# Kernel tuning notes

Hardware: AMD Instinct MI355X
Metric: run time of the kernel (lower is better)

The kernel has to match this reference:

```python
import jax, jax.numpy as jnp
import numpy as np

EMB, GCN = 256, 256
N_REL = 200
B, E, TOPK = 256, 100000, 64
N_PREV, N_ENT, N_TIME = 50000, 20000, 2000


def _linear(x, w, b):
    # torch nn.Linear convention: w is [out, in]
    return x @ w.T + b


def setup_inputs() -> dict:
    key = jax.random.key(0)
    ks = jax.random.split(key, 32)
    nrm = lambda k, s: (jax.random.normal(k, s, jnp.float32) * 0.05)
    # facts columns: b, n, h, r, t, ts. b built so every batch has >= TOPK facts.
    b_col = jax.random.permutation(ks[0], jnp.arange(E, dtype=jnp.int32) % B)
    n_col = jax.random.randint(ks[1], (E,), 0, N_PREV, jnp.int32)
    h_col = jax.random.randint(ks[2], (E,), 0, N_ENT, jnp.int32)
    r_col = jax.random.randint(ks[3], (E,), 0, N_REL, jnp.int32)  # r+1 indexes [zero;rel]
    t_col = jax.random.randint(ks[4], (E,), 0, N_ENT, jnp.int32)
    ts_col = jax.random.randint(ks[5], (E,), 0, N_TIME, jnp.int32)
    facts = jnp.stack([b_col, n_col, h_col, r_col, t_col, ts_col], axis=1)
    return {
        "query_time": jax.random.randint(ks[6], (B,), 0, N_TIME, jnp.int32),  # unused by forward
        "query_emd": nrm(ks[7], (B, EMB)),
        "temp_neighbors_facts": facts,
        "ent_emd": nrm(ks[8], (N_ENT, GCN)),
        "rel_emd": nrm(ks[9], (N_REL, GCN)),
        "hidden_node": nrm(ks[10], (N_PREV, EMB)),
        "hidden_rel": nrm(ks[11], (N_PREV, EMB)),
        "hidden_time": nrm(ks[12], (N_PREV, EMB)),  # unused by forward
        "att_agg": jax.random.uniform(ks[13], (N_PREV,), jnp.float32),
        "time_emd": nrm(ks[14], (N_TIME, EMB)),
        "zero_rel_emd": nrm(ks[15], (1, GCN)),
        "W_message_w": nrm(ks[16], (EMB, 2 * EMB)), "W_message_b": jnp.zeros((EMB,), jnp.float32),
        "att_1_w": nrm(ks[17], (1, 3 * EMB)), "att_1_b": jnp.zeros((1,), jnp.float32),
        "att_2_w": nrm(ks[18], (1, EMB)), "att_2_b": jnp.zeros((1,), jnp.float32),
        "W_h_w": nrm(ks[19], (EMB, 2 * EMB)), "W_h_b": jnp.zeros((EMB,), jnp.float32),
        "lin_e_ts_w": nrm(ks[20], (EMB, GCN + EMB)), "lin_e_ts_b": jnp.zeros((EMB,), jnp.float32),
        "lin_r_ts_w": nrm(ks[21], (EMB, GCN)), "lin_r_ts_b": jnp.zeros((EMB,), jnp.float32),
        "lin_time_w": nrm(ks[22], (EMB, EMB)), "lin_time_b": jnp.zeros((EMB,), jnp.float32),
        "gru_w_ih": nrm(ks[23], (3 * EMB, EMB)), "gru_w_hh": nrm(ks[24], (3 * EMB, EMB)),
        "gru_b_ih": jnp.zeros((3 * EMB,), jnp.float32), "gru_b_hh": jnp.zeros((3 * EMB,), jnp.float32),
        "batch_size": B, "device": 0, "max_nodes": TOPK,
    }


def reference(query_time, query_emd, temp_neighbors_facts, ent_emd, rel_emd,
              hidden_node, hidden_rel, hidden_time, att_agg, time_emd,
              zero_rel_emd, W_message_w, W_message_b, att_1_w, att_1_b,
              att_2_w, att_2_b, W_h_w, W_h_b, lin_e_ts_w, lin_e_ts_b,
              lin_r_ts_w, lin_r_ts_b, lin_time_w, lin_time_b,
              gru_w_ih, gru_w_hh, gru_b_ih, gru_b_hh,
              batch_size, device, max_nodes):
    f = temp_neighbors_facts
    b, n, r, t, ts = f[:, 0], f[:, 1], f[:, 3], f[:, 4], f[:, 5]

    hidden_node_pre = hidden_node[n]            # [E, EMB]
    hidden_rel_pre = hidden_rel[n]              # [E, EMB]
    rel_all = jnp.concatenate([zero_rel_emd, rel_emd], axis=0)
    h_r = rel_all[r + 1]                        # [E, GCN]
    h_ts_raw = time_emd[ts]                     # [E, EMB]
    h_t = _linear(jnp.concatenate([ent_emd[t], h_ts_raw], -1), lin_e_ts_w, lin_e_ts_b)
    h_r = _linear(h_r, lin_r_ts_w, lin_r_ts_b)
    _ = _linear(h_ts_raw, lin_time_w, lin_time_b)  # computed but unused in original

    message = _linear(jnp.concatenate([hidden_node_pre, h_r], -1), W_message_w, W_message_b)
    att_input = jnp.concatenate([query_emd[b], message, h_t], -1)  # [E, 3*EMB]
    att1 = jax.nn.sigmoid(_linear(att_input, att_1_w, att_1_b))[:, 0]

    # single-step GRU (torch nn.GRU gate math)
    gi = h_r @ gru_w_ih.T + gru_b_ih            # [E, 3*EMB]
    gh = hidden_rel_pre @ gru_w_hh.T + gru_b_hh
    i_r, i_z, i_n = jnp.split(gi, 3, axis=-1)
    h_rg, h_zg, h_ng = jnp.split(gh, 3, axis=-1)
    rg = jax.nn.sigmoid(i_r + h_rg)
    zg = jax.nn.sigmoid(i_z + h_zg)
    ng = jnp.tanh(i_n + rg * h_ng)
    hidden_rel_new = (1.0 - zg) * ng + zg * hidden_rel_pre

    att2 = jax.nn.sigmoid(_linear(hidden_rel_new, att_2_w, att_2_b))[:, 0]
    attention = (att1 + att2) * 0.5

    # vectorized per-batch top-k (each batch is guaranteed >= max_nodes facts)
    order = jnp.lexsort((-attention, b))        # sort by batch asc, attention desc
    counts = jax.ops.segment_sum(jnp.ones_like(b), b, num_segments=batch_size)
    starts = jnp.cumsum(counts) - counts
    sel = (starts[:, None] + jnp.arange(max_nodes)[None, :]).reshape(-1)
    new_index = order[sel]                      # [B*topk]

    facts_k = f[new_index]
    message = message[new_index]
    hidden_rel_new = hidden_rel_new[new_index]
    attention = (att1[new_index] + att2[new_index]) * 0.5
    b_k, n_k = facts_k[:, 0], facts_k[:, 1]
    attention = attention * att_agg[n_k]
    M = b_k.shape[0]

    rows = facts_k[:, jnp.array([0, 4, 5])]     # (b, t, ts)
    tail_nodes, tail_index = jnp.unique(rows, axis=0, size=M, fill_value=0, return_inverse=True)
    tail_index = tail_index.reshape(-1)

    tail_emd = _linear(jnp.concatenate([ent_emd[tail_nodes[:, 1]], time_emd[tail_nodes[:, 2]]], -1),
                       lin_e_ts_w, lin_e_ts_b)

    # group_max_norm: normalize attention by per-batch sum (0/0 -> 0)
    den = jax.ops.segment_sum(attention, b_k, num_segments=batch_size)[b_k]
    safe_den = jnp.where(den != 0, den, 1.0)
    attention = jnp.where(den != 0, attention / safe_den, 0.0)

    message_agg = jax.ops.segment_sum(attention[:, None] * message, tail_index, num_segments=M)
    hidden_node_new = _linear(jnp.concatenate([message_agg, tail_emd], -1), W_h_w, W_h_b)  # act = identity
    hidden_rel_out = jax.ops.segment_sum(attention[:, None] * hidden_rel_new, tail_index, num_segments=M)
    att_agg_new = jax.ops.segment_sum(attention, tail_index, num_segments=M)
    return tail_nodes, hidden_node_new, hidden_rel_out, att_agg_new
```

## Files before the change

kernel.cpp:

```cpp
#include <hip/hip_runtime.h>
#include <hip/hip_bf16.h>

#define E_N    100000
#define B_N    256
#define TOPK   64
#define NPREV  50000
#define NENT   20000
#define NTIME  2000
#define NREL   200
#define M_OUT  16384
#define NT8    6250

static __device__ __forceinline__ float sigm(float x){ return 1.f/(1.f+expf(-x)); }

__global__ void zero_kernel(unsigned* __restrict__ p, int n){
  int i = blockIdx.x*256 + threadIdx.x;
  if (i < n) p[i] = 0u;
}

__global__ void pack_w_kernel(const float* __restrict__ w_msg,
                              const float* __restrict__ w_hh,
                              const float* __restrict__ lets_w,
                              const float* __restrict__ w_h,
                              float4* __restrict__ wP,
                              float4* __restrict__ wPL,
                              float4* __restrict__ wPH){
  int i = blockIdx.x*256 + threadIdx.x;
  if (i < 65536){
    int t = i & 255, mat = (i >> 8) & 3, kblk = i >> 10;
    float4 v;
    if (mat == 0) v = *(const float4*)&w_msg[(size_t)t*512 + kblk*4];
    else          v = *(const float4*)&w_hh[(size_t)((mat-1)*256 + t)*256 + kblk*4];
    wP[i] = v;
  } else if (i < 98304){
    int j = i - 65536;
    int t = j & 255, mat = (j >> 8) & 1, kblk = j >> 9;
    wPL[j] = *(const float4*)&lets_w[(size_t)t*512 + mat*256 + kblk*4];
  } else if (i < 131072){
    int j = i - 98304;
    int t = j & 255, kblk = j >> 8;
    wPH[j] = *(const float4*)&w_h[(size_t)t*512 + kblk*4];
  }
}

__global__ void matvec_fused(const float* __restrict__ w_msg,
                             const float* __restrict__ lets_w,
                             const float* __restrict__ lets_b,
                             const float* __restrict__ att1w,
                             const float* __restrict__ att1b,
                             float* __restrict__ wm1a, float* __restrict__ ve,
                             float* __restrict__ vts, float* __restrict__ consts){
  int blk = blockIdx.x, t = threadIdx.x;
  if (blk == 3){
    if (t < 64){
      float p = 0.f;
      for (int d = t; d < 256; d += 64) p += lets_b[d]*att1w[512+d];
      for (int o = 32; o > 0; o >>= 1) p += __shfl_down(p, o);
      if (t == 0) consts[0] = att1b[0] + p;
    }
    return;
  }
  const float* M; int moff; const float* v; float* out;
  if (blk == 0){ M = w_msg;  moff = 0;   v = att1w+256; out = wm1a; }
  else if (blk == 1){ M = lets_w; moff = 0;   v = att1w+512; out = ve; }
  else { M = lets_w; moff = 256; v = att1w+512; out = vts; }
  float acc = 0.f;
  #pragma unroll 8
  for (int d = 0; d < 256; ++d) acc += M[(size_t)d*512 + moff + t] * v[d];
  out[t] = acc;
}

__global__ void rows_dot_multi(
    const float* __restrict__ A0, const float* __restrict__ v0, float* __restrict__ o0, int n0,
    const float* __restrict__ A1, const float* __restrict__ v1, float* __restrict__ o1_, int n1,
    const float* __restrict__ A2, const float* __restrict__ v2, float* __restrict__ o2, int n2,
    const float* __restrict__ A3, const float* __restrict__ v3, float* __restrict__ o3, int n3,
    const float* __restrict__ A4, const float* __restrict__ v4, float* __restrict__ o4, int n4){
  int gid = blockIdx.x*256 + threadIdx.x;
  int wid = gid >> 6, lane = gid & 63;
  const float* A; const float* v; float* o; int r;
  if (wid < n0){ A=A0; v=v0; o=o0; r=wid; }
  else if ((wid -= n0) < n1){ A=A1; v=v1; o=o1_; r=wid; }
  else if ((wid -= n1) < n2){ A=A2; v=v2; o=o2; r=wid; }
  else if ((wid -= n2) < n3){ A=A3; v=v3; o=o3; r=wid; }
  else if ((wid -= n3) < n4){ A=A4; v=v4; o=o4; r=wid; }
  else return;
  const float* row = A + (size_t)r*256;
  float p = 0.f;
  for (int k = lane; k < 256; k += 64) p += row[k]*v[k];
  for (int off = 32; off > 0; off >>= 1) p += __shfl_down(p, off);
  if (lane == 0) o[r] = p;
}

template<int ND>
__global__ __launch_bounds__(256) void tile_linear(
    const float* __restrict__ A, int lda,
    const float* __restrict__ Bw, int ldb, int boff,
    const float* __restrict__ bias,
    float* __restrict__ out, int ldo, int rows){
  __shared__ float a_s[16][260];
  int tile0 = blockIdx.x*16;
  for (int idx = threadIdx.x; idx < 16*256; idx += 256){
    int i = idx >> 8, k = idx & 255;
    int row = tile0 + i;
    a_s[i][k] = (row < rows) ? A[(size_t)row*lda + k] : 0.f;
  }
  __syncthreads();
  int d = threadIdx.x;
  const float* brow[ND];
  #pragma unroll
  for (int q = 0; q < ND; ++q) brow[q] = Bw + (size_t)(d + 256*q)*ldb + boff;
  float acc[ND][16];
  #pragma unroll
  for (int q = 0; q < ND; ++q){
    float bv = bias ? bias[d + 256*q] : 0.f;
    #pragma unroll
    for (int i = 0; i < 16; ++i) acc[q][i] = bv;
  }
  for (int k = 0; k < 256; k += 4){
    float4 w[ND];
    #pragma unroll
    for (int q = 0; q < ND; ++q) w[q] = *(const float4*)(brow[q] + k);
    #pragma unroll
    for (int i = 0; i < 16; ++i){
      float4 a = *(const float4*)&a_s[i][k];
      #pragma unroll
      for (int q = 0; q < ND; ++q)
        acc[q][i] += w[q].x*a.x + w[q].y*a.y + w[q].z*a.z + w[q].w*a.w;
    }
  }
  #pragma unroll
  for (int i = 0; i < 16; ++i){
    int row = tile0 + i;
    if (row < rows){
      #pragma unroll
      for (int q = 0; q < ND; ++q) out[(size_t)row*ldo + d + 256*q] = acc[q][i];
    }
  }
}

__global__ __launch_bounds__(256) void gemv_ets2(
    const float* __restrict__ ent_emd, const float* __restrict__ time_emd,
    const float4* __restrict__ wPL, const float* __restrict__ lets_b,
    float* __restrict__ ent_t, float* __restrict__ time_t){
  int blk = blockIdx.x, t = threadIdx.x;
  const float* act; float* out; int matsel, tile0; float bv;
  if (blk < NENT/16){
    act = ent_emd; out = ent_t; matsel = 0; tile0 = blk*16; bv = lets_b[t];
  } else {
    act = time_emd; out = time_t; matsel = 1; tile0 = (blk - NENT/16)*16; bv = 0.f;
  }
  float acc[16];
  #pragma unroll
  for (int p = 0; p < 16; ++p) acc[p] = bv;
  float4 w = wPL[matsel*256 + t];
  for (int kb = 0; kb < 64; ++kb){
    int kbn = (kb + 1) & 63;
    float4 nw = wPL[(kbn*2 + matsel)*256 + t];
    int k = kb*4;
    #pragma unroll
    for (int p = 0; p < 16; ++p){
      float4 a = *(const float4*)&act[(size_t)(tile0+p)*256 + k];
      acc[p] += w.x*a.x + w.y*a.y + w.z*a.z + w.w*a.w;
    }
    w = nw;
  }
  #pragma unroll
  for (int p = 0; p < 16; ++p)
    out[(size_t)(tile0+p)*256 + t] = acc[p];
}

__global__ void hist2_kernel(const int* __restrict__ facts,
                             int* __restrict__ cnt_t, int* __restrict__ cnt_b){
  int e = blockIdx.x*256 + threadIdx.x;
  if (e < E_N){
    atomicAdd(&cnt_t[facts[e*6+1] >> 3], 1);
    atomicAdd(&cnt_b[facts[e*6+0]], 1);
  }
}

__global__ __launch_bounds__(256) void scan2_lds(
    const int* __restrict__ cnt_t, int* __restrict__ off_t, int* __restrict__ cur_t,
    const int* __restrict__ cnt_b, int* __restrict__ off_b, int* __restrict__ cur_b){
  __shared__ int buf[6272];
  __shared__ int sums[256];
  int t = threadIdx.x;
  int c0 = t*25, c1 = c0 + 25; if (c1 > NT8) c1 = NT8; if (c0 > NT8) c0 = NT8;
  int s = 0;
  for (int i = c0; i < c1; ++i){ buf[i] = s; s += cnt_t[i]; }
  sums[t] = s;
  __syncthreads();
  for (int o = 1; o < 256; o <<= 1){
    int v = (t >= o) ? sums[t-o] : 0;
    __syncthreads();
    sums[t] += v;
    __syncthreads();
  }
  int add = (t == 0) ? 0 : sums[t-1];
  for (int i = c0; i < c1; ++i){ int v = buf[i] + add; off_t[i] = v; cur_t[i] = v; }
  if (t == 0) off_t[NT8] = E_N;
  __syncthreads();
  int orig = cnt_b[t];
  sums[t] = orig;
  __syncthreads();
  for (int o = 1; o < 256; o <<= 1){
    int v = (t >= o) ? sums[t-o] : 0;
    __syncthreads();
    sums[t] += v;
    __syncthreads();
  }
  int ex = sums[t] - orig;
  off_b[t] = ex; cur_b[t] = ex;
  if (t == 0) off_b[B_N] = E_N;
}

__global__ void scatter2_kernel(const int* __restrict__ facts,
                                int* __restrict__ cur_t, int* __restrict__ edges_t,
                                int* __restrict__ cur_b, int* __restrict__ edges_b){
  int e = blockIdx.x*256 + threadIdx.x;
  if (e < E_N){
    int pt = atomicAdd(&cur_t[facts[e*6+1] >> 3], 1);
    edges_t[pt] = e;
    int pb = atomicAdd(&cur_b[facts[e*6+0]], 1);
    edges_b[pb] = e;
  }
}

__global__ __launch_bounds__(256) void att_kernel(
    const float* __restrict__ hidden_rel,
    const float4* __restrict__ wP,
    const float* __restrict__ b_hh,
    const float* __restrict__ gi,
    const float* __restrict__ att2w, const float* __restrict__ att2b,
    const int* __restrict__ facts,
    const int* __restrict__ bin_off, const int* __restrict__ bin_edges,
    const float* __restrict__ qdot, const float* __restrict__ sn_m,
    const float* __restrict__ sr_m, const float* __restrict__ se,
    const float* __restrict__ st,   const float* __restrict__ consts,
    float* __restrict__ attention){
  __shared__ float gh_s[8][776];
  int tile0 = blockIdx.x*8;
  int t = threadIdx.x;

  float acc[3][8];
  #pragma unroll
  for (int q = 0; q < 3; ++q)
    #pragma unroll
    for (int p = 0; p < 8; ++p) acc[q][p] = 0.f;

  float4 w1 = wP[256 + t], w2 = wP[512 + t], w3 = wP[768 + t];
  for (int kb = 0; kb < 64; ++kb){
    int kbn = (kb + 1) & 63;
    int nb = (kbn*4)*256 + t;
    float4 nw1 = wP[nb + 256], nw2 = wP[nb + 512], nw3 = wP[nb + 768];
    int k = kb*4;
    #pragma unroll
    for (int p = 0; p < 8; ++p){
      float4 a = *(const float4*)&hidden_rel[(size_t)(tile0+p)*256 + k];
      acc[0][p] += w1.x*a.x + w1.y*a.y + w1.z*a.z + w1.w*a.w;
      acc[1][p] += w2.x*a.x + w2.y*a.y + w2.z*a.z + w2.w*a.w;
      acc[2][p] += w3.x*a.x + w3.y*a.y + w3.z*a.z + w3.w*a.w;
    }
    w1 = nw1; w2 = nw2; w3 = nw3;
  }
  #pragma unroll
  for (int q = 0; q < 3; ++q){
    float bv = b_hh[t + 256*q];
    #pragma unroll
    for (int p = 0; p < 8; ++p)
      gh_s[p][t + 256*q] = acc[q][p] + bv;
  }
  __syncthreads();

  int wv = t >> 6, l = t & 63;
  int o0 = bin_off[blockIdx.x], o1 = bin_off[blockIdx.x + 1];
  int d0 = 4*l;
  float4 a2 = *(const float4*)&att2w[d0];
  float c1 = consts[0];
  float a2b = att2b[0];
  for (int idx = o0 + wv; idx < o1; idx += 4){
    int e  = bin_edges[idx];
    int b  = facts[e*6+0], n = facts[e*6+1], r = facts[e*6+3];
    int t_ = facts[e*6+4], ts_ = facts[e*6+5];
    int nl = n - tile0;
    float4 ghr = *(const float4*)&gh_s[nl][d0];
    float4 ghz = *(const float4*)&gh_s[nl][256+d0];
    float4 ghn = *(const float4*)&gh_s[nl][512+d0];
    const float* girow = gi + (size_t)r*768;
    float4 gir = *(const float4*)&girow[d0];
    float4 giz = *(const float4*)&girow[256+d0];
    float4 gin = *(const float4*)&girow[512+d0];
    float4 hp  = *(const float4*)&hidden_rel[(size_t)n*256 + d0];
    float partial;
    {
      float rg = sigm(gir.x + ghr.x), zg = sigm(giz.x + ghz.x);
      float ng = tanhf(gin.x + rg*ghn.x);
      partial = a2.x * ((1.f - zg)*ng + zg*hp.x);
    }{
      float rg = sigm(gir.y + ghr.y), zg = sigm(giz.y + ghz.y);
      float ng = tanhf(gin.y + rg*ghn.y);
      partial += a2.y * ((1.f - zg)*ng + zg*hp.y);
    }{
      float rg = sigm(gir.z + ghr.z), zg = sigm(giz.z + ghz.z);
      float ng = tanhf(gin.z + rg*ghn.z);
      partial += a2.z * ((1.f - zg)*ng + zg*hp.z);
    }{
      float rg = sigm(gir.w + ghr.w), zg = sigm(giz.w + ghz.w);
      float ng = tanhf(gin.w + rg*ghn.w);
      partial += a2.w * ((1.f - zg)*ng + zg*hp.w);
    }
    #pragma unroll
    for (int o = 32; o > 0; o >>= 1) partial += __shfl_xor(partial, o);
    if (l == 0){
      float att2 = sigm(partial + a2b);
      float x1 = qdot[b] + sn_m[n] + sr_m[r] + se[t_] + st[ts_] + c1;
      attention[e] = 0.5f*(sigm(x1) + att2);
    }
  }
}

__global__ __launch_bounds__(256) void topk_kernel(
    const int* __restrict__ facts, const float* __restrict__ attention,
    const float* __restrict__ att_agg,
    const int* __restrict__ boff, const int* __restrict__ bedges,
    int* __restrict__ sel_edge, float* __restrict__ att_norm,
    unsigned* __restrict__ skey, int* __restrict__ Ub){
  __shared__ float sa[512];
  __shared__ int   si[512];
  __shared__ unsigned sk[64];
  int b = blockIdx.x, tid = threadIdx.x;
  sa[tid] = -1.f; sa[tid+256] = -1.f;
  si[tid] = 0x7fffffff; si[tid+256] = 0x7fffffff;
  __syncthreads();
  int o0 = boff[b], cnt = boff[b+1] - o0;
  for (int i = tid; i < cnt; i += 256){
    int e = bedges[o0 + i];
    sa[i] = attention[e]; si[i] = e;
  }
  __syncthreads();
  for (int k = 2; k <= 512; k <<= 1){
    for (int j = k >> 1; j > 0; j >>= 1){
      for (int i0 = tid; i0 < 512; i0 += 256){
        int l = i0 ^ j;
        if (l > i0){
          float ai = sa[i0], al = sa[l];
          int   ii = si[i0], il = si[l];
          bool lFirst = (al > ai) || (al == ai && il < ii);
          bool up = ((i0 & k) == 0);
          if (up ? lFirst : !lFirst){
            sa[i0] = al; sa[l] = ai; si[i0] = il; si[l] = ii;
          }
        }
      }
      __syncthreads();
    }
  }
  if (tid < 64){
    int e = si[tid];
    bool valid = (e != 0x7fffffff);
    if (!valid) e = 0;
    int n = facts[e*6+1];
    float a = valid ? sa[tid]*att_agg[n] : 0.f;
    float den = a;
    for (int o = 32; o > 0; o >>= 1) den += __shfl_down(den, o);
    den = __shfl(den, 0);
    float norm = (den != 0.f) ? a/den : 0.f;
    sel_edge[b*64 + tid] = e;
    att_norm[b*64 + tid] = norm;
    int t_ = facts[e*6+4], ts_ = facts[e*6+5];
    unsigned key = (((unsigned)t_) << 11) | (unsigned)ts_;
    sk[tid] = (key << 6) | (unsigned)tid;
  }
  __syncthreads();
  for (int k = 2; k <= 64; k <<= 1){
    for (int j = k >> 1; j > 0; j >>= 1){
      unsigned nv = 0; bool act = tid < 64;
      if (act){
        unsigned mine = sk[tid], other = sk[tid ^ j];
        bool up = ((tid & k) == 0);
        bool keepmin = (up == ((tid & j) == 0));
        nv = keepmin ? (mine < other ? mine : other) : (mine > other ? mine : other);
      }
      __syncthreads();
      if (act) sk[tid] = nv;
      __syncthreads();
    }
  }
  if (tid < 64){
    unsigned kk = sk[tid];
    skey[b*64 + tid] = kk;
    bool head = (tid == 0) || ((kk >> 6) != (sk[tid-1] >> 6));
    unsigned long long bal = __ballot(head);
    if (tid == 0) Ub[b] = __popcll(bal);
  }
}

__global__ void offs_scan_kernel(const int* __restrict__ Ub, int* __restrict__ offs){
  int lane = threadIdx.x;
  int run = 0;
  for (int base = 0; base < 256; base += 64){
    int orig = Ub[base + lane];
    int v = orig;
    for (int o = 1; o < 64; o <<= 1){ int t = __shfl_up(v, o); if (lane >= o) v += t; }
    offs[base + lane] = run + v - orig;
    run += __shfl(v, 63);
  }
  if (lane == 0) offs[256] = run;
}

__global__ void emit_kernel(const unsigned* __restrict__ skey, const int* __restrict__ offs,
                            int* __restrict__ us, int* __restrict__ tails,
                            float* __restrict__ out_tail){
  int b = blockIdx.x, tid = threadIdx.x;
  unsigned kk = skey[b*64 + tid];
  bool head = (tid == 0) || ((kk >> 6) != (skey[b*64 + tid - 1] >> 6));
  unsigned long long bal = __ballot(head);
  unsigned long long mask_le = (tid == 63) ? ~0ull : ((1ull << (tid+1)) - 1ull);
  int ulocal = __popcll(bal & mask_le) - 1;
  int u = offs[b] + ulocal;
  us[b*64 + tid] = u;
  if (head){
    unsigned key = kk >> 6;
    int t_ = (int)(key >> 11), ts_ = (int)(key & 2047u);
    tails[u*3+0] = b; tails[u*3+1] = t_; tails[u*3+2] = ts_;
    out_tail[u*3+0] = (float)b;
    out_tail[u*3+1] = (float)t_;
    out_tail[u*3+2] = (float)ts_;
  }
}

__global__ __launch_bounds__(256) void sel_kernel(
    const unsigned* __restrict__ skey, const int* __restrict__ sel_edge,
    const float* __restrict__ att_norm, const int* __restrict__ facts,
    const float* __restrict__ hidden_node, const float* __restrict__ hidden_rel,
    const float4* __restrict__ wP,
    const float* __restrict__ msg_r, const float* __restrict__ gi,
    const float* __restrict__ b_hh,
    float* __restrict__ msg_sel, float* __restrict__ hrn_sel){
  __shared__ int n_s[16], r_s[16];
  __shared__ float av_s[16];
  int base = blockIdx.x*16;
  int t = threadIdx.x;
  if (t < 16){
    int gs = base + t;
    int b = gs >> 6, i = gs & 63;
    int j = (int)(skey[(size_t)b*64 + i] & 63u);
    int s = b*64 + j;
    int e = sel_edge[s];
    n_s[t] = facts[e*6+1];
    r_s[t] = facts[e*6+3];
    av_s[t] = att_norm[s];
  }
  __syncthreads();

  float accM[16], accR[16], accZ[16], accN[16];
  #pragma unroll
  for (int e = 0; e < 16; ++e){ accM[e]=0.f; accR[e]=0.f; accZ[e]=0.f; accN[e]=0.f; }

  for (int kb = 0; kb < 64; ++kb){
    int nb = (kb*4)*256 + t;
    float4 w0 = wP[nb], w1 = wP[nb + 256], w2 = wP[nb + 512], w3 = wP[nb + 768];
    int k = kb*4;
    #pragma unroll
    for (int e = 0; e < 16; ++e){
      float4 an = *(const float4*)&hidden_node[(size_t)n_s[e]*256 + k];
      float4 ah = *(const float4*)&hidden_rel[(size_t)n_s[e]*256 + k];
      accM[e] += w0.x*an.x + w0.y*an.y + w0.z*an.z + w0.w*an.w;
      accR[e] += w1.x*ah.x + w1.y*ah.y + w1.z*ah.z + w1.w*ah.w;
      accZ[e] += w2.x*ah.x + w2.y*ah.y + w2.z*ah.z + w2.w*ah.w;
      accN[e] += w3.x*ah.x + w3.y*ah.y + w3.z*ah.z + w3.w*ah.w;
    }
  }

  float bhr = b_hh[t], bhz = b_hh[256+t], bhn = b_hh[512+t];
  #pragma unroll
  for (int e = 0; e < 16; ++e){
    int r = r_s[e]; float a = av_s[e];
    const float* girow = gi + (size_t)r*768;
    float msgv = accM[e] + msg_r[(size_t)r*256 + t];
    float rg = sigm(girow[t]      + accR[e] + bhr);
    float zg = sigm(girow[256+t]  + accZ[e] + bhz);
    float ng = tanhf(girow[512+t] + rg*(accN[e] + bhn));
    float hp = hidden_rel[(size_t)n_s[e]*256 + t];
    float hrn = (1.f - zg)*ng + zg*hp;
    size_t o = (size_t)(base + e)*256 + t;
    msg_sel[o] = a*msgv;
    hrn_sel[o] = a*hrn;
  }
}

__global__ __launch_bounds__(256) void segsum_kernel(
    const unsigned* __restrict__ skey, const int* __restrict__ us,
    const float* __restrict__ att_norm,
    const float* __restrict__ msg_sel, const float* __restrict__ hrn_sel,
    float* __restrict__ msg_agg, float* __restrict__ out_hrel,
    float* __restrict__ out_aagg){
  int b = blockIdx.x, d = threadIdx.x;
  float accm = 0.f, acch = 0.f, acca = 0.f;
  int ucur = -1;
  for (int i = 0; i < 64; ++i){
    int u = us[b*64 + i];
    if (u != ucur){
      if (ucur >= 0){
        msg_agg[(size_t)ucur*256 + d] = accm;
        out_hrel[(size_t)ucur*256 + d] = acch;
        if (d == 0) out_aagg[ucur] = acca;
      }
      ucur = u; accm = 0.f; acch = 0.f; acca = 0.f;
    }
    size_t o = (size_t)(b*64 + i)*256 + d;
    accm += msg_sel[o];
    acch += hrn_sel[o];
    int j = (int)(skey[b*64 + i] & 63u);
    acca += att_norm[b*64 + j];
  }
  if (ucur >= 0){
    msg_agg[(size_t)ucur*256 + d] = accm;
    out_hrel[(size_t)ucur*256 + d] = acch;
    if (d == 0) out_aagg[ucur] = acca;
  }
}

__global__ __launch_bounds__(256) void final_kernel(
    const float* __restrict__ msg_agg, const int* __restrict__ tails,
    const float* __restrict__ ent_t, const float* __restrict__ time_t,
    const float4* __restrict__ wPH,
    const float* __restrict__ b_h,
    float* __restrict__ out_hn){
  int tile0 = blockIdx.x*16, t = threadIdx.x;
  int tu[16], tsu[16];
  #pragma unroll
  for (int p = 0; p < 16; ++p){
    tu[p]  = tails[(tile0+p)*3+1];
    tsu[p] = tails[(tile0+p)*3+2];
  }
  float acc[16];
  float bv = b_h[t];
  #pragma unroll
  for (int p = 0; p < 16; ++p) acc[p] = bv;
  float4 w = wPH[t];
  for (int kb = 0; kb < 128; ++kb){
    int kbn = (kb + 1) & 127;
    float4 nw = wPH[kbn*256 + t];
    if (kb < 64){
      int k = kb*4;
      #pragma unroll
      for (int p = 0; p < 16; ++p){
        float4 a = *(const float4*)&msg_agg[(size_t)(tile0+p)*256 + k];
        acc[p] += w.x*a.x + w.y*a.y + w.z*a.z + w.w*a.w;
      }
    } else {
      int k = (kb-64)*4;
      #pragma unroll
      for (int p = 0; p < 16; ++p){
        float4 a1 = *(const float4*)&ent_t[(size_t)tu[p]*256 + k];
        float4 a2 = *(const float4*)&time_t[(size_t)tsu[p]*256 + k];
        float ax = a1.x + a2.x, ay = a1.y + a2.y, az = a1.z + a2.z, aw = a1.w + a2.w;
        acc[p] += w.x*ax + w.y*ay + w.z*az + w.w*aw;
      }
    }
    w = nw;
  }
  #pragma unroll
  for (int p = 0; p < 16; ++p)
    out_hn[(size_t)(tile0+p)*256 + t] = acc[p];
}

extern "C" void kernel_launch(void* const* d_in, const int* in_sizes, int n_in,
                              void* d_out, int out_size, void* d_ws, size_t ws_size,
                              hipStream_t stream){
  const float* query_emd   = (const float*)d_in[1];
  const int*   facts       = (const int*)  d_in[2];
  const float* ent_emd     = (const float*)d_in[3];
  const float* rel_emd     = (const float*)d_in[4];
  const float* hidden_node = (const float*)d_in[5];
  const float* hidden_rel  = (const float*)d_in[6];
  const float* att_agg     = (const float*)d_in[8];
  const float* time_emd    = (const float*)d_in[9];
  const float* w_msg       = (const float*)d_in[11];
  const float* b_msg       = (const float*)d_in[12];
  const float* att1w       = (const float*)d_in[13];
  const float* att1b       = (const float*)d_in[14];
  const float* att2w       = (const float*)d_in[15];
  const float* att2b       = (const float*)d_in[16];
  const float* w_h         = (const float*)d_in[17];
  const float* b_h         = (const float*)d_in[18];
  const float* lets_w      = (const float*)d_in[19];
  const float* lets_b      = (const float*)d_in[20];
  const float* lrts_w      = (const float*)d_in[21];
  const float* lrts_b      = (const float*)d_in[22];
  const float* w_ih        = (const float*)d_in[25];
  const float* w_hh        = (const float*)d_in[26];
  const float* b_ih        = (const float*)d_in[27];
  const float* b_hh        = (const float*)d_in[28];

  char* p = (char*)d_ws;
  auto alloc = [&](size_t bytes) -> void* {
    void* r = (void*)p; p += (bytes + 255) & ~(size_t)255; return r;
  };
  char* zstart = p;
  int* bin_cnt  = (int*)alloc(6272*4);
  int* bin_cur  = (int*)alloc(6272*4);
  int* bcnt     = (int*)alloc(256*4);
  int* bcur     = (int*)alloc(256*4);
  int* tails    = (int*)alloc((size_t)M_OUT*3*4);
  float* msg_agg= (float*)alloc((size_t)M_OUT*256*4);
  size_t zero_words = (size_t)(p - zstart)/4;
  float* msg_sel= (float*)alloc((size_t)M_OUT*256*4);
  float* hrn_sel= (float*)alloc((size_t)M_OUT*256*4);
  float* ent_t  = (float*)alloc((size_t)NENT*256*4);
  float* time_t = (float*)alloc((size_t)NTIME*256*4);
  int* bin_off  = (int*)alloc(6272*4);
  int* bin_edges= (int*)alloc(E_N*4);
  int* boff     = (int*)alloc(257*4);
  int* bedges   = (int*)alloc(E_N*4);
  float* attention = (float*)alloc(E_N*4);
  float* qdot   = (float*)alloc(256*4);
  float* sn_m   = (float*)alloc(NPREV*4);
  float* se     = (float*)alloc(NENT*4);
  float* st     = (float*)alloc(NTIME*4);
  float* sr_m   = (float*)alloc(NREL*4);
  float* wm1a   = (float*)alloc(256*4);
  float* ve     = (float*)alloc(256*4);
  float* vts    = (float*)alloc(256*4);
  float* consts = (float*)alloc(8*4);
  float* hr2    = (float*)alloc((size_t)NREL*256*4);
  float* msg_r  = (float*)alloc((size_t)NREL*256*4);
  float* gi     = (float*)alloc((size_t)NREL*768*4);
  float4* wP    = (float4*)alloc((size_t)65536*16);
  float4* wPL   = (float4*)alloc((size_t)32768*16);
  float4* wPH   = (float4*)alloc((size_t)32768*16);
  int* sel_edge = (int*)alloc(M_OUT*4);
  float* att_nrm= (float*)alloc(M_OUT*4);
  unsigned* skey= (unsigned*)alloc(M_OUT*4);
  int* Ub       = (int*)alloc(256*4);
  int* offs     = (int*)alloc(257*4);
  int* us       = (int*)alloc(M_OUT*4);
  (void)ws_size; (void)in_sizes; (void)n_in;

  float* out_f     = (float*)d_out;
  float* out_tail  = out_f;
  float* out_hn    = out_f + (size_t)M_OUT*3;
  float* out_hrel  = out_f + (size_t)M_OUT*3 + (size_t)M_OUT*256;
  float* out_aagg  = out_f + (size_t)M_OUT*3 + (size_t)2*M_OUT*256;

  zero_kernel<<<(out_size+255)/256, 256, 0, stream>>>((unsigned*)d_out, out_size);
  zero_kernel<<<((int)zero_words+255)/256, 256, 0, stream>>>((unsigned*)zstart, (int)zero_words);

  pack_w_kernel<<<512, 256, 0, stream>>>(w_msg, w_hh, lets_w, w_h, wP, wPL, wPH);
  matvec_fused<<<4, 256, 0, stream>>>(w_msg, lets_w, lets_b, att1w, att1b, wm1a, ve, vts, consts);

  tile_linear<1><<<(NREL+15)/16, 256, 0, stream>>>(rel_emd, 256, lrts_w, 256, 0, lrts_b, hr2, 256, NREL);
  tile_linear<1><<<(NREL+15)/16, 256, 0, stream>>>(hr2, 256, w_msg, 512, 256, b_msg, msg_r, 256, NREL);
  tile_linear<3><<<(NREL+15)/16, 256, 0, stream>>>(hr2, 256, w_ih, 256, 0, b_ih, gi, 768, NREL);

  gemv_ets2<<<NENT/16 + NTIME/16, 256, 0, stream>>>(ent_emd, time_emd, wPL, lets_b, ent_t, time_t);

  {
    int total_rows = B_N + NPREV + NENT + NTIME + NREL;
    int blocks = (total_rows*64 + 255)/256;
    rows_dot_multi<<<blocks, 256, 0, stream>>>(
        query_emd, att1w, qdot, B_N,
        hidden_node, wm1a, sn_m, NPREV,
        ent_emd, ve, se, NENT,
        time_emd, vts, st, NTIME,
        msg_r, att1w+256, sr_m, NREL);
  }

  hist2_kernel<<<(E_N+255)/256, 256, 0, stream>>>(facts, bin_cnt, bcnt);
  scan2_lds<<<1, 256, 0, stream>>>(bin_cnt, bin_off, bin_cur, bcnt, boff, bcur);
  scatter2_kernel<<<(E_N+255)/256, 256, 0, stream>>>(facts, bin_cur, bin_edges, bcur, bedges);

  att_kernel<<<NT8, 256, 0, stream>>>(hidden_rel, wP, b_hh, gi, att2w, att2b,
      facts, bin_off, bin_edges, qdot, sn_m, sr_m, se, st, consts, attention);

  topk_kernel<<<B_N, 256, 0, stream>>>(facts, attention, att_agg, boff, bedges,
      sel_edge, att_nrm, skey, Ub);
  offs_scan_kernel<<<1, 64, 0, stream>>>(Ub, offs);
  emit_kernel<<<B_N, 64, 0, stream>>>(skey, offs, us, tails, out_tail);
  sel_kernel<<<M_OUT/16, 256, 0, stream>>>(skey, sel_edge, att_nrm, facts,
      hidden_node, hidden_rel, wP, msg_r, gi, b_hh, msg_sel, hrn_sel);
  segsum_kernel<<<B_N, 256, 0, stream>>>(skey, us, att_nrm, msg_sel, hrn_sel,
      msg_agg, out_hrel, out_aagg);
  final_kernel<<<M_OUT/16, 256, 0, stream>>>(msg_agg, tails, ent_t, time_t, wPH, b_h, out_hn);
}
```

Measured before the change: 1.242 ms.

## Fuse setup kernels, chain relation linears, drop weight prefetch, scalarize row pointers

Merges the two zero kernels into one launch, and the weight-pack and matvec kernels into one. Chains the three relation-side linears plus the sr_m dot into a single kernel that keeps the intermediate in shared memory, which removes the hr2 buffer and several launches. It also removes manual software prefetch of weights in several loops and precomputes wave-uniform row pointers with readfirstlane so the gather addresses become scalar. These cut launch overhead and address arithmetic. In exchange the weight loads lose their explicit prefetch, and the relation chain runs on only 13 blocks.

```diff
diff --git a/kernel.cpp b/kernel.cpp
--- a/kernel.cpp
+++ b/kernel.cpp
@@ -13,45 +13,47 @@
 
 static __device__ __forceinline__ float sigm(float x){ return 1.f/(1.f+expf(-x)); }
 
-__global__ void zero_kernel(unsigned* __restrict__ p, int n){
+__global__ void zero2_kernel(unsigned* __restrict__ p1, int n1,
+                             unsigned* __restrict__ p2, int n2){
   int i = blockIdx.x*256 + threadIdx.x;
-  if (i < n) p[i] = 0u;
-}
-
-__global__ void pack_w_kernel(const float* __restrict__ w_msg,
-                              const float* __restrict__ w_hh,
-                              const float* __restrict__ lets_w,
-                              const float* __restrict__ w_h,
-                              float4* __restrict__ wP,
-                              float4* __restrict__ wPL,
-                              float4* __restrict__ wPH){
-  int i = blockIdx.x*256 + threadIdx.x;
-  if (i < 65536){
-    int t = i & 255, mat = (i >> 8) & 3, kblk = i >> 10;
-    float4 v;
-    if (mat == 0) v = *(const float4*)&w_msg[(size_t)t*512 + kblk*4];
-    else          v = *(const float4*)&w_hh[(size_t)((mat-1)*256 + t)*256 + kblk*4];
-    wP[i] = v;
-  } else if (i < 98304){
-    int j = i - 65536;
-    int t = j & 255, mat = (j >> 8) & 1, kblk = j >> 9;
-    wPL[j] = *(const float4*)&lets_w[(size_t)t*512 + mat*256 + kblk*4];
-  } else if (i < 131072){
-    int j = i - 98304;
-    int t = j & 255, kblk = j >> 8;
-    wPH[j] = *(const float4*)&w_h[(size_t)t*512 + kblk*4];
-  }
-}
-
-__global__ void matvec_fused(const float* __restrict__ w_msg,
-                             const float* __restrict__ lets_w,
-                             const float* __restrict__ lets_b,
-                             const float* __restrict__ att1w,
-                             const float* __restrict__ att1b,
-                             float* __restrict__ wm1a, float* __restrict__ ve,
-                             float* __restrict__ vts, float* __restrict__ consts){
+  if (i < n1) p1[i] = 0u;
+  else if (i < n1 + n2) p2[i - n1] = 0u;
+}
+
+__global__ void pack_matvec(const float* __restrict__ w_msg,
+                            const float* __restrict__ w_hh,
+                            const float* __restrict__ lets_w,
+                            const float* __restrict__ w_h,
+                            const float* __restrict__ lets_b,
+                            const float* __restrict__ att1w,
+                            const float* __restrict__ att1b,
+                            float4* __restrict__ wP,
+                            float4* __restrict__ wPL,
+                            float4* __restrict__ wPH,
+                            float* __restrict__ wm1a, float* __restrict__ ve,
+                            float* __restrict__ vts, float* __restrict__ consts){
   int blk = blockIdx.x, t = threadIdx.x;
-  if (blk == 3){
+  if (blk < 512){
+    int i = blk*256 + t;
+    if (i < 65536){
+      int tt = i & 255, mat = (i >> 8) & 3, kblk = i >> 10;
+      float4 v;
+      if (mat == 0) v = *(const float4*)&w_msg[(size_t)tt*512 + kblk*4];
+      else          v = *(const float4*)&w_hh[(size_t)((mat-1)*256 + tt)*256 + kblk*4];
+      wP[i] = v;
+    } else if (i < 98304){
+      int j = i - 65536;
+      int tt = j & 255, mat = (j >> 8) & 1, kblk = j >> 9;
+      wPL[j] = *(const float4*)&lets_w[(size_t)tt*512 + mat*256 + kblk*4];
+    } else {
+      int j = i - 98304;
+      int tt = j & 255, kblk = j >> 8;
+      wPH[j] = *(const float4*)&w_h[(size_t)tt*512 + kblk*4];
+    }
+    return;
+  }
+  int sub = blk - 512;
+  if (sub == 3){
     if (t < 64){
       float p = 0.f;
       for (int d = t; d < 256; d += 64) p += lets_b[d]*att1w[512+d];
@@ -61,8 +63,8 @@
     return;
   }
   const float* M; int moff; const float* v; float* out;
-  if (blk == 0){ M = w_msg;  moff = 0;   v = att1w+256; out = wm1a; }
-  else if (blk == 1){ M = lets_w; moff = 0;   v = att1w+512; out = ve; }
+  if (sub == 0){ M = w_msg;  moff = 0;   v = att1w+256; out = wm1a; }
+  else if (sub == 1){ M = lets_w; moff = 0;   v = att1w+512; out = ve; }
   else { M = lets_w; moff = 256; v = att1w+512; out = vts; }
   float acc = 0.f;
   #pragma unroll 8
@@ -74,8 +76,7 @@
     const float* __restrict__ A0, const float* __restrict__ v0, float* __restrict__ o0, int n0,
     const float* __restrict__ A1, const float* __restrict__ v1, float* __restrict__ o1_, int n1,
     const float* __restrict__ A2, const float* __restrict__ v2, float* __restrict__ o2, int n2,
-    const float* __restrict__ A3, const float* __restrict__ v3, float* __restrict__ o3, int n3,
-    const float* __restrict__ A4, const float* __restrict__ v4, float* __restrict__ o4, int n4){
+    const float* __restrict__ A3, const float* __restrict__ v3, float* __restrict__ o3, int n3){
   int gid = blockIdx.x*256 + threadIdx.x;
   int wid = gid >> 6, lane = gid & 63;
   const float* A; const float* v; float* o; int r;
@@ -83,7 +84,6 @@
   else if ((wid -= n0) < n1){ A=A1; v=v1; o=o1_; r=wid; }
   else if ((wid -= n1) < n2){ A=A2; v=v2; o=o2; r=wid; }
   else if ((wid -= n2) < n3){ A=A3; v=v3; o=o3; r=wid; }
-  else if ((wid -= n3) < n4){ A=A4; v=v4; o=o4; r=wid; }
   else return;
   const float* row = A + (size_t)r*256;
   float p = 0.f;
@@ -92,50 +92,107 @@
   if (lane == 0) o[r] = p;
 }
 
-template<int ND>
-__global__ __launch_bounds__(256) void tile_linear(
-    const float* __restrict__ A, int lda,
-    const float* __restrict__ Bw, int ldb, int boff,
-    const float* __restrict__ bias,
-    float* __restrict__ out, int ldo, int rows){
+__global__ __launch_bounds__(256) void rel_chain(
+    const float* __restrict__ rel_emd,
+    const float* __restrict__ lrts_w, const float* __restrict__ lrts_b,
+    const float* __restrict__ w_msg,  const float* __restrict__ b_msg,
+    const float* __restrict__ w_ih,   const float* __restrict__ b_ih,
+    const float* __restrict__ att1w,
+    float* __restrict__ msg_r, float* __restrict__ gi, float* __restrict__ sr_m){
   __shared__ float a_s[16][260];
+  __shared__ float h_s[16][260];
   int tile0 = blockIdx.x*16;
-  for (int idx = threadIdx.x; idx < 16*256; idx += 256){
+  int t = threadIdx.x;
+  for (int idx = t; idx < 16*256; idx += 256){
     int i = idx >> 8, k = idx & 255;
     int row = tile0 + i;
-    a_s[i][k] = (row < rows) ? A[(size_t)row*lda + k] : 0.f;
-  }
-  __syncthreads();
-  int d = threadIdx.x;
-  const float* brow[ND];
-  #pragma unroll
-  for (int q = 0; q < ND; ++q) brow[q] = Bw + (size_t)(d + 256*q)*ldb + boff;
-  float acc[ND][16];
-  #pragma unroll
-  for (int q = 0; q < ND; ++q){
-    float bv = bias ? bias[d + 256*q] : 0.f;
-    #pragma unroll
-    for (int i = 0; i < 16; ++i) acc[q][i] = bv;
-  }
-  for (int k = 0; k < 256; k += 4){
-    float4 w[ND];
-    #pragma unroll
-    for (int q = 0; q < ND; ++q) w[q] = *(const float4*)(brow[q] + k);
+    a_s[i][k] = (row < NREL) ? rel_emd[(size_t)row*256 + k] : 0.f;
+  }
+  __syncthreads();
+  {
+    const float* brow = lrts_w + (size_t)t*256;
+    float acc[16];
+    float bv = lrts_b[t];
+    #pragma unroll
+    for (int i = 0; i < 16; ++i) acc[i] = bv;
+    for (int k = 0; k < 256; k += 4){
+      float4 w = *(const float4*)(brow + k);
+      #pragma unroll
+      for (int i = 0; i < 16; ++i){
+        float4 a = *(const float4*)&a_s[i][k];
+        acc[i] += w.x*a.x + w.y*a.y + w.z*a.z + w.w*a.w;
+      }
+    }
+    __syncthreads();
+    #pragma unroll
+    for (int i = 0; i < 16; ++i) h_s[i][t] = acc[i];
+  }
+  __syncthreads();
+  float accm[16];
+  {
+    const float* brow = w_msg + (size_t)t*512 + 256;
+    float bv = b_msg[t];
+    #pragma unroll
+    for (int i = 0; i < 16; ++i) accm[i] = bv;
+    for (int k = 0; k < 256; k += 4){
+      float4 w = *(const float4*)(brow + k);
+      #pragma unroll
+      for (int i = 0; i < 16; ++i){
+        float4 a = *(const float4*)&h_s[i][k];
+        accm[i] += w.x*a.x + w.y*a.y + w.z*a.z + w.w*a.w;
+      }
+    }
     #pragma unroll
     for (int i = 0; i < 16; ++i){
-      float4 a = *(const float4*)&a_s[i][k];
+      int row = tile0 + i;
+      if (row < NREL) msg_r[(size_t)row*256 + t] = accm[i];
+    }
+  }
+  {
+    float accg[3][16];
+    #pragma unroll
+    for (int q = 0; q < 3; ++q){
+      float bv = b_ih[t + 256*q];
       #pragma unroll
-      for (int q = 0; q < ND; ++q)
-        acc[q][i] += w[q].x*a.x + w[q].y*a.y + w[q].z*a.z + w[q].w*a.w;
-    }
-  }
-  #pragma unroll
-  for (int i = 0; i < 16; ++i){
+      for (int i = 0; i < 16; ++i) accg[q][i] = bv;
+    }
+    const float* b0 = w_ih + (size_t)t*256;
+    const float* b1 = w_ih + (size_t)(256+t)*256;
+    const float* b2 = w_ih + (size_t)(512+t)*256;
+    for (int k = 0; k < 256; k += 4){
+      float4 w0 = *(const float4*)(b0 + k);
+      float4 w1 = *(const float4*)(b1 + k);
+      float4 w2 = *(const float4*)(b2 + k);
+      #pragma unroll
+      for (int i = 0; i < 16; ++i){
+        float4 a = *(const float4*)&h_s[i][k];
+        accg[0][i] += w0.x*a.x + w0.y*a.y + w0.z*a.z + w0.w*a.w;
+        accg[1][i] += w1.x*a.x + w1.y*a.y + w1.z*a.z + w1.w*a.w;
+        accg[2][i] += w2.x*a.x + w2.y*a.y + w2.z*a.z + w2.w*a.w;
+      }
+    }
+    #pragma unroll
+    for (int i = 0; i < 16; ++i){
+      int row = tile0 + i;
+      if (row < NREL){
+        #pragma unroll
+        for (int q = 0; q < 3; ++q)
+          gi[(size_t)row*768 + t + 256*q] = accg[q][i];
+      }
+    }
+  }
+  __syncthreads();
+  float a1 = att1w[256 + t];
+  #pragma unroll
+  for (int i = 0; i < 16; ++i) a_s[i][t] = accm[i]*a1;
+  __syncthreads();
+  int wv = t >> 6, l = t & 63;
+  for (int i = wv*4; i < wv*4 + 4; ++i){
+    float p = a_s[i][l] + a_s[i][l+64] + a_s[i][l+128] + a_s[i][l+192];
+    #pragma unroll
+    for (int o = 32; o > 0; o >>= 1) p += __shfl_xor(p, o);
     int row = tile0 + i;
-    if (row < rows){
-      #pragma unroll
-      for (int q = 0; q < ND; ++q) out[(size_t)row*ldo + d + 256*q] = acc[q][i];
-    }
+    if (l == 0 && row < NREL) sr_m[row] = p;
   }
 }
 
@@ -153,17 +210,14 @@
   float acc[16];
   #pragma unroll
   for (int p = 0; p < 16; ++p) acc[p] = bv;
-  float4 w = wPL[matsel*256 + t];
   for (int kb = 0; kb < 64; ++kb){
-    int kbn = (kb + 1) & 63;
-    float4 nw = wPL[(kbn*2 + matsel)*256 + t];
+    float4 w = wPL[(kb*2 + matsel)*256 + t];
     int k = kb*4;
     #pragma unroll
     for (int p = 0; p < 16; ++p){
       float4 a = *(const float4*)&act[(size_t)(tile0+p)*256 + k];
       acc[p] += w.x*a.x + w.y*a.y + w.z*a.z + w.w*a.w;
     }
-    w = nw;
   }
   #pragma unroll
   for (int p = 0; p < 16; ++p)
@@ -248,11 +302,9 @@
     #pragma unroll
     for (int p = 0; p < 8; ++p) acc[q][p] = 0.f;
 
-  float4 w1 = wP[256 + t], w2 = wP[512 + t], w3 = wP[768 + t];
   for (int kb = 0; kb < 64; ++kb){
-    int kbn = (kb + 1) & 63;
-    int nb = (kbn*4)*256 + t;
-    float4 nw1 = wP[nb + 256], nw2 = wP[nb + 512], nw3 = wP[nb + 768];
+    int nb = (kb*4)*256 + t;
+    float4 w1 = wP[nb + 256], w2 = wP[nb + 512], w3 = wP[nb + 768];
     int k = kb*4;
     #pragma unroll
     for (int p = 0; p < 8; ++p){
@@ -261,7 +313,6 @@
       acc[1][p] += w2.x*a.x + w2.y*a.y + w2.z*a.z + w2.w*a.w;
       acc[2][p] += w3.x*a.x + w3.y*a.y + w3.z*a.z + w3.w*a.w;
     }
-    w1 = nw1; w2 = nw2; w3 = nw3;
   }
   #pragma unroll
   for (int q = 0; q < 3; ++q){
@@ -453,6 +504,15 @@
   }
   __syncthreads();
 
+  const float* pn[16];
+  const float* ph[16];
+  #pragma unroll
+  for (int e = 0; e < 16; ++e){
+    int ne = __builtin_amdgcn_readfirstlane(n_s[e]);
+    pn[e] = hidden_node + (size_t)ne*256;
+    ph[e] = hidden_rel  + (size_t)ne*256;
+  }
+
   float accM[16], accR[16], accZ[16], accN[16];
   #pragma unroll
   for (int e = 0; e < 16; ++e){ accM[e]=0.f; accR[e]=0.f; accZ[e]=0.f; accN[e]=0.f; }
@@ -463,8 +523,8 @@
     int k = kb*4;
     #pragma unroll
     for (int e = 0; e < 16; ++e){
-      float4 an = *(const float4*)&hidden_node[(size_t)n_s[e]*256 + k];
-      float4 ah = *(const float4*)&hidden_rel[(size_t)n_s[e]*256 + k];
+      float4 an = *(const float4*)(pn[e] + k);
+      float4 ah = *(const float4*)(ph[e] + k);
       accM[e] += w0.x*an.x + w0.y*an.y + w0.z*an.z + w0.w*an.w;
       accR[e] += w1.x*ah.x + w1.y*ah.y + w1.z*ah.z + w1.w*ah.w;
       accZ[e] += w2.x*ah.x + w2.y*ah.y + w2.z*ah.z + w2.w*ah.w;
@@ -481,7 +541,7 @@
     float rg = sigm(girow[t]      + accR[e] + bhr);
     float zg = sigm(girow[256+t]  + accZ[e] + bhz);
     float ng = tanhf(girow[512+t] + rg*(accN[e] + bhn));
-    float hp = hidden_rel[(size_t)n_s[e]*256 + t];
+    float hp = ph[e][t];
     float hrn = (1.f - zg)*ng + zg*hp;
     size_t o = (size_t)(base + e)*256 + t;
     msg_sel[o] = a*msgv;
@@ -528,20 +588,21 @@
     const float* __restrict__ b_h,
     float* __restrict__ out_hn){
   int tile0 = blockIdx.x*16, t = threadIdx.x;
-  int tu[16], tsu[16];
+  const float* pe[16];
+  const float* pt_[16];
   #pragma unroll
   for (int p = 0; p < 16; ++p){
-    tu[p]  = tails[(tile0+p)*3+1];
-    tsu[p] = tails[(tile0+p)*3+2];
+    int tu  = __builtin_amdgcn_readfirstlane(tails[(tile0+p)*3+1]);
+    int tsu = __builtin_amdgcn_readfirstlane(tails[(tile0+p)*3+2]);
+    pe[p]  = ent_t  + (size_t)tu*256;
+    pt_[p] = time_t + (size_t)tsu*256;
   }
   float acc[16];
   float bv = b_h[t];
   #pragma unroll
   for (int p = 0; p < 16; ++p) acc[p] = bv;
-  float4 w = wPH[t];
   for (int kb = 0; kb < 128; ++kb){
-    int kbn = (kb + 1) & 127;
-    float4 nw = wPH[kbn*256 + t];
+    float4 w = wPH[kb*256 + t];
     if (kb < 64){
       int k = kb*4;
       #pragma unroll
@@ -553,13 +614,12 @@
       int k = (kb-64)*4;
       #pragma unroll
       for (int p = 0; p < 16; ++p){
-        float4 a1 = *(const float4*)&ent_t[(size_t)tu[p]*256 + k];
-        float4 a2 = *(const float4*)&time_t[(size_t)tsu[p]*256 + k];
+        float4 a1 = *(const float4*)(pe[p] + k);
+        float4 a2 = *(const float4*)(pt_[p] + k);
         float ax = a1.x + a2.x, ay = a1.y + a2.y, az = a1.z + a2.z, aw = a1.w + a2.w;
         acc[p] += w.x*ax + w.y*ay + w.z*az + w.w*aw;
       }
     }
-    w = nw;
   }
   #pragma unroll
   for (int p = 0; p < 16; ++p)
@@ -624,7 +684,6 @@
   float* ve     = (float*)alloc(256*4);
   float* vts    = (float*)alloc(256*4);
   float* consts = (float*)alloc(8*4);
-  float* hr2    = (float*)alloc((size_t)NREL*256*4);
   float* msg_r  = (float*)alloc((size_t)NREL*256*4);
   float* gi     = (float*)alloc((size_t)NREL*768*4);
   float4* wP    = (float4*)alloc((size_t)65536*16);
@@ -644,27 +703,28 @@
   float* out_hrel  = out_f + (size_t)M_OUT*3 + (size_t)M_OUT*256;
   float* out_aagg  = out_f + (size_t)M_OUT*3 + (size_t)2*M_OUT*256;
 
-  zero_kernel<<<(out_size+255)/256, 256, 0, stream>>>((unsigned*)d_out, out_size);
-  zero_kernel<<<((int)zero_words+255)/256, 256, 0, stream>>>((unsigned*)zstart, (int)zero_words);
-
-  pack_w_kernel<<<512, 256, 0, stream>>>(w_msg, w_hh, lets_w, w_h, wP, wPL, wPH);
-  matvec_fused<<<4, 256, 0, stream>>>(w_msg, lets_w, lets_b, att1w, att1b, wm1a, ve, vts, consts);
-
-  tile_linear<1><<<(NREL+15)/16, 256, 0, stream>>>(rel_emd, 256, lrts_w, 256, 0, lrts_b, hr2, 256, NREL);
-  tile_linear<1><<<(NREL+15)/16, 256, 0, stream>>>(hr2, 256, w_msg, 512, 256, b_msg, msg_r, 256, NREL);
-  tile_linear<3><<<(NREL+15)/16, 256, 0, stream>>>(hr2, 256, w_ih, 256, 0, b_ih, gi, 768, NREL);
+  {
+    int ntot = out_size + (int)zero_words;
+    zero2_kernel<<<(ntot+255)/256, 256, 0, stream>>>(
+        (unsigned*)d_out, out_size, (unsigned*)zstart, (int)zero_words);
+  }
+
+  pack_matvec<<<516, 256, 0, stream>>>(w_msg, w_hh, lets_w, w_h, lets_b, att1w, att1b,
+      wP, wPL, wPH, wm1a, ve, vts, consts);
+
+  rel_chain<<<(NREL+15)/16, 256, 0, stream>>>(rel_emd, lrts_w, lrts_b,
+      w_msg, b_msg, w_ih, b_ih, att1w, msg_r, gi, sr_m);
 
   gemv_ets2<<<NENT/16 + NTIME/16, 256, 0, stream>>>(ent_emd, time_emd, wPL, lets_b, ent_t, time_t);
 
   {
-    int total_rows = B_N + NPREV + NENT + NTIME + NREL;
+    int total_rows = B_N + NPREV + NENT + NTIME;
     int blocks = (total_rows*64 + 255)/256;
     rows_dot_multi<<<blocks, 256, 0, stream>>>(
         query_emd, att1w, qdot, B_N,
         hidden_node, wm1a, sn_m, NPREV,
         ent_emd, ve, se, NENT,
-        time_emd, vts, st, NTIME,
-        msg_r, att1w+256, sr_m, NREL);
+        time_emd, vts, st, NTIME);
   }
 
   hist2_kernel<<<(E_N+255)/256, 256, 0, stream>>>(facts, bin_cnt, bcnt);
```

New measurement: 1.208 ms. 1.03x faster.
